# Kernel optimization log

Hardware: AMD Instinct MI355X
Metric: run time of the kernel (lower is better)

The kernel has to match this reference:

```python
import jax, jax.numpy as jnp
import numpy as np

NUM_HEADS = 4
HIDDEN = 384

def _l2norm(t, eps=1e-12):
    # torch.nn.functional.normalize(dim=-1): x / max(||x||_2, eps)
    n = jnp.sqrt(jnp.sum(t * t, axis=-1, keepdims=True))
    return t / jnp.maximum(n, eps)

def setup_inputs() -> dict:
    key = jax.random.key(0)
    k1, k2, k3, k4 = jax.random.split(key, 4)
    B, N, C = 4, 16384, HIDDEN
    x = jax.random.normal(k1, (B, N, C), dtype=jnp.float32)
    W_qkv = jax.random.normal(k2, (3 * C, C), dtype=jnp.float32) * 0.02  # torch Linear weight [out,in], no bias
    temperature_ch = jnp.ones((NUM_HEADS, 1, 1), dtype=jnp.float32)
    W_out = jax.random.normal(k3, (C, C), dtype=jnp.float32) * 0.02
    b_out = jax.random.normal(k4, (C,), dtype=jnp.float32) * 0.02
    return {"x": x, "W_qkv": W_qkv, "temperature_ch": temperature_ch,
            "W_out": W_out, "b_out": b_out,
            "B_in": 4, "C_in": C, "H": 32, "W": 32, "D": 16}

def reference(x, W_qkv, temperature_ch, W_out, b_out, B_in, C_in, H, W, D):
    B, N, C = x.shape
    h = NUM_HEADS
    d = C // h
    # qkv projection: (B,N,3C) -> (3,B,h,N,d)
    qkv = (x @ W_qkv.T).reshape(B, N, 3, h, d).transpose(2, 0, 3, 1, 4)
    q, k, v = qkv[0], qkv[1], qkv[2]
    # transpose token/channel axes: (B,h,d,N)
    q = jnp.swapaxes(q, -2, -1)
    k = jnp.swapaxes(k, -2, -1)
    v = jnp.swapaxes(v, -2, -1)
    # L2-normalize over tokens (last axis)
    q = _l2norm(q)
    k = _l2norm(k)
    # channel attention: (B,h,d,d)
    attn = jnp.einsum('bhcn,bhdn->bhcd', q, k)
    attn = attn * temperature_ch  # (h,1,1) broadcasts over (B,h,d,d)
    attn = jax.nn.softmax(attn, axis=-1)
    # (B,h,d,N) -> (B,N,h,d) -> (B,N,C)
    x_CA = jnp.einsum('bhcd,bhdn->bhcn', attn, v)
    x_CA = x_CA.transpose(0, 3, 1, 2).reshape(B, N, C)
    return x_CA @ W_out.T + b_out
```

## Files before the change

### kernel.cpp

```cpp
#include <hip/hip_runtime.h>
#include <math.h>


#define B_    4
#define NTOK  16384
#define C_    384
#define NH    4
#define DH    96

typedef __attribute__((ext_vector_type(8))) short short8;
typedef __attribute__((ext_vector_type(4))) float f32x4;
typedef __attribute__((ext_vector_type(4))) unsigned short ushort4v;
typedef __attribute__((ext_vector_type(8))) unsigned short ushort8v;

#define XH_B   0ull
#define XHT_B  50331648ull
#define GP_B   100663296ull
#define G_B    138412032ull
#define P_B    140771328ull
#define SSQ_B  145489920ull
#define ATT_B  145502208ull
#define T_B    146092032ull
#define MP_B   148451328ull
#define MPH_B  150810624ull
#define WS_NEED 151990272ull

#define FG_OFF    0
#define FG_SZ     (B_*C_*C_)
#define FP_OFF    (FG_OFF + FG_SZ)
#define FP_SZ     (2*B_*C_*C_)
#define FSSQ_OFF  (FP_OFF + FP_SZ)
#define FSSQ_SZ   (2*B_*C_)
#define FATT_OFF  (FSSQ_OFF + FSSQ_SZ)
#define FATT_SZ   (B_*NH*DH*DH)
#define FT_OFF    (FATT_OFF + FATT_SZ)
#define FT_SZ     (B_*C_*C_)
#define FMP_OFF   (FT_OFF + FT_SZ)

__device__ inline unsigned short f2bf(float f) {
    unsigned u = __float_as_uint(f);
    u += 0x7FFFu + ((u >> 16) & 1u);
    return (unsigned short)(u >> 16);
}

__device__ inline void load16(const void* g, void* l) {
    __builtin_amdgcn_global_load_lds(
        (const __attribute__((address_space(1))) unsigned int*)g,
        (__attribute__((address_space(3))) unsigned int*)l, 16, 0, 0);
}

__global__ __launch_bounds__(256) void k_conv(const float* __restrict__ X,
                                              unsigned short* __restrict__ Xh,
                                              unsigned short* __restrict__ XhT) {
    __shared__ __align__(16) unsigned short Th[64][72];
    const int tid = threadIdx.x;
    const int t0 = blockIdx.x * 64, c0 = blockIdx.y * 64, b = blockIdx.z;
    const int tl0 = tid >> 4, cl = (tid & 15) * 4;
#pragma unroll
    for (int p = 0; p < 4; ++p) {
        const int t = t0 + tl0 + p * 16;
        const float4 v = *(const float4*)(X + ((size_t)(b * NTOK + t)) * C_ + c0 + cl);
        const unsigned short h0 = f2bf(v.x), h1 = f2bf(v.y), h2 = f2bf(v.z), h3 = f2bf(v.w);
        ushort4v hv; hv.x = h0; hv.y = h1; hv.z = h2; hv.w = h3;
        *(ushort4v*)(Xh + ((size_t)(b * NTOK + t)) * C_ + c0 + cl) = hv;
        const int tl = tl0 + p * 16;
        Th[cl + 0][tl] = h0; Th[cl + 1][tl] = h1; Th[cl + 2][tl] = h2; Th[cl + 3][tl] = h3;
    }
    __syncthreads();
    const int c = tid >> 2, seg = (tid & 3) * 16;
    const ushort8v a  = *(const ushort8v*)&Th[c][seg];
    const ushort8v bb = *(const ushort8v*)&Th[c][seg + 8];
    unsigned short* dst = XhT + ((size_t)(b * C_ + c0 + c)) * NTOK + t0 + seg;
    *(ushort8v*)dst       = a;
    *(ushort8v*)(dst + 8) = bb;
}

__global__ __launch_bounds__(256, 2) void k_gram_mfma(const unsigned short* __restrict__ XhT,
                                                      float* __restrict__ Gpart) {
    __shared__ __align__(16) unsigned char sm[32768];
    const int l = blockIdx.x;
    const int xcd = l & 7, slot = l >> 3;
    const int grp = xcd * 8 + slot / 9, tile = slot % 9;
    const int chunk = grp >> 2, b = grp & 3;
    const int ti = tile / 3, tj = tile % 3;
    const int tid = threadIdx.x;
    const int lane = tid & 63, wid = tid >> 6;
    const int wr = wid >> 1, wc = wid & 1;

    const int e = (lane & 7) ^ (lane >> 3);
    const int rsub = lane >> 3;

    const size_t rowb = (size_t)NTOK * 2;
    const unsigned char* Abase = (const unsigned char*)XhT + (size_t)(b * C_ + ti * 128) * rowb;
    const unsigned char* Bbase = (const unsigned char*)XhT + (size_t)(b * C_ + tj * 128) * rowb;

    f32x4 acc[4][4];
#pragma unroll
    for (int i = 0; i < 4; i++)
#pragma unroll
        for (int j = 0; j < 4; j++) acc[i][j] = (f32x4)(0.f);

    for (int ks = 0; ks < 16; ++ks) {
        const size_t colb = (size_t)(chunk * 1024 + ks * 64) * 2 + (size_t)e * 16;
        __syncthreads();
#pragma unroll
        for (int call = 0; call < 4; ++call) {
            const int row = wid * 32 + call * 8 + rsub;
            load16(Abase + (size_t)row * rowb + colb, sm + (wid * 32 + call * 8) * 128);
            load16(Bbase + (size_t)row * rowb + colb, sm + 16384 + (wid * 32 + call * 8) * 128);
        }
        __syncthreads();
#pragma unroll
        for (int p = 0; p < 2; ++p) {
            const int s = p * 4 + (lane >> 4);
            short8 av[4], bv[4];
#pragma unroll
            for (int fi = 0; fi < 4; ++fi) {
                const int c = wr * 64 + fi * 16 + (lane & 15);
                av[fi] = *(const short8*)(sm + c * 128 + ((s ^ (c & 7)) << 4));
            }
#pragma unroll
            for (int fj = 0; fj < 4; ++fj) {
                const int c = wc * 64 + fj * 16 + (lane & 15);
                bv[fj] = *(const short8*)(sm + 16384 + c * 128 + ((s ^ (c & 7)) << 4));
            }
#pragma unroll
            for (int fi = 0; fi < 4; ++fi)
#pragma unroll
                for (int fj = 0; fj < 4; ++fj)
                    acc[fi][fj] = __builtin_amdgcn_mfma_f32_16x16x32_bf16(av[fi], bv[fj], acc[fi][fj], 0, 0, 0);
        }
    }
    float* gp = Gpart + (size_t)grp * (C_ * C_);
    const int r0 = (lane >> 4) * 4, cc = lane & 15;
#pragma unroll
    for (int fi = 0; fi < 4; ++fi) {
        const int ci = ti * 128 + wr * 64 + fi * 16 + r0;
#pragma unroll
        for (int fj = 0; fj < 4; ++fj) {
            const int cj = tj * 128 + wc * 64 + fj * 16 + cc;
#pragma unroll
            for (int r = 0; r < 4; ++r)
                gp[(size_t)(ci + r) * C_ + cj] = acc[fi][fj][r];
        }
    }
}

__global__ __launch_bounds__(256) void k_reduceG(const float* __restrict__ Gpart,
                                                 float* __restrict__ G) {
    const size_t eo = ((size_t)blockIdx.x * 256 + threadIdx.x) * 4;
    float4 s = *(const float4*)(Gpart + eo);
#pragma unroll
    for (int c = 1; c < 16; ++c) {
        const float4 v = *(const float4*)(Gpart + (size_t)c * (B_ * C_ * C_) + eo);
        s.x += v.x; s.y += v.y; s.z += v.z; s.w += v.w;
    }
    *(float4*)(G + eo) = s;
}

__global__ __launch_bounds__(256) void k_convM(const float* __restrict__ Mp,
                                               unsigned short* __restrict__ Mph) {
    const size_t eo = ((size_t)blockIdx.x * 256 + threadIdx.x) * 4;
    const float4 v = *(const float4*)(Mp + eo);
    ushort4v h; h.x = f2bf(v.x); h.y = f2bf(v.y); h.z = f2bf(v.z); h.w = f2bf(v.w);
    *(ushort4v*)(Mph + eo) = h;
}

__global__ __launch_bounds__(256, 2) void k_out_mfma(const unsigned short* __restrict__ Xh,
                                                     const unsigned short* __restrict__ Mph,
                                                     const float* __restrict__ bias,
                                                     float* __restrict__ out) {
    __shared__ __align__(16) unsigned char sm[32768];
    const int l = blockIdx.x;
    const int xcd = l & 7, k = l >> 3;
    const int mblk = xcd * 64 + k / 3, nblk = k % 3;
    const int m0 = mblk * 128, i0 = nblk * 128;
    const int b = mblk >> 7;
    const int tid = threadIdx.x;
    const int lane = tid & 63, wid = tid >> 6;
    const int wr = wid >> 1, wc = wid & 1;

    const int e = (lane & 7) ^ (lane >> 3);
    const int rsub = lane >> 3;

    const unsigned char* Abase = (const unsigned char*)Xh + (size_t)m0 * (C_ * 2);
    const unsigned char* Bbase = (const unsigned char*)Mph + (size_t)b * (C_ * C_ * 2) + (size_t)i0 * (C_ * 2);

    f32x4 acc[4][4];
#pragma unroll
    for (int i = 0; i < 4; i++)
#pragma unroll
        for (int j = 0; j < 4; j++) acc[i][j] = (f32x4)(0.f);

    for (int ks = 0; ks < 6; ++ks) {
        const size_t colb = (size_t)ks * 128 + (size_t)e * 16;
        __syncthreads();
#pragma unroll
        for (int call = 0; call < 4; ++call) {
            const int row = wid * 32 + call * 8 + rsub;
            load16(Abase + (size_t)row * (C_ * 2) + colb, sm + (wid * 32 + call * 8) * 128);
            load16(Bbase + (size_t)row * (C_ * 2) + colb, sm + 16384 + (wid * 32 + call * 8) * 128);
        }
        __syncthreads();
#pragma unroll
        for (int p = 0; p < 2; ++p) {
            const int s = p * 4 + (lane >> 4);
            short8 av[4], bv[4];
#pragma unroll
            for (int fi = 0; fi < 4; ++fi) {
                const int c = wr * 64 + fi * 16 + (lane & 15);
                av[fi] = *(const short8*)(sm + c * 128 + ((s ^ (c & 7)) << 4));
            }
#pragma unroll
            for (int fj = 0; fj < 4; ++fj) {
                const int c = wc * 64 + fj * 16 + (lane & 15);
                bv[fj] = *(const short8*)(sm + 16384 + c * 128 + ((s ^ (c & 7)) << 4));
            }
#pragma unroll
            for (int fi = 0; fi < 4; ++fi)
#pragma unroll
                for (int fj = 0; fj < 4; ++fj)
                    acc[fi][fj] = __builtin_amdgcn_mfma_f32_16x16x32_bf16(av[fi], bv[fj], acc[fi][fj], 0, 0, 0);
        }
    }
    const int r0 = (lane >> 4) * 4, cc = lane & 15;
#pragma unroll
    for (int fi = 0; fi < 4; ++fi) {
        const int m = m0 + wr * 64 + fi * 16 + r0;
#pragma unroll
        for (int fj = 0; fj < 4; ++fj) {
            const int ii = i0 + wc * 64 + fj * 16 + cc;
            const float bi = bias[ii];
#pragma unroll
            for (int r = 0; r < 4; ++r)
                out[(size_t)(m + r) * C_ + ii] = acc[fi][fj][r] + bi;
        }
    }
}

__global__ __launch_bounds__(256) void k_zero(float* __restrict__ p, int n) {
    int i = blockIdx.x * 256 + threadIdx.x;
    if (i < n) p[i] = 0.f;
}

__global__ __launch_bounds__(256, 2) void k_P(const float* __restrict__ Wqkv,
                                              const float* __restrict__ G,
                                              float* __restrict__ P) {
    __shared__ float As[16][132];
    __shared__ float Bs[16][132];
    const int tid = threadIdx.x;
    const int sel = blockIdx.z & 1, b = blockIdx.z >> 1;
    const int m0 = blockIdx.x * 128, n0 = blockIdx.y * 128;
    const float* A  = Wqkv + (size_t)sel * C_ * C_;
    const float* Bm = G + (size_t)b * C_ * C_;
    const int lr = tid >> 1, lk = (tid & 1) * 8;
    const int tm = (tid & 15) * 8, tn = (tid >> 4) * 8;
    float acc[8][8];
#pragma unroll
    for (int i = 0; i < 8; i++)
#pragma unroll
        for (int j = 0; j < 8; j++) acc[i][j] = 0.f;

    for (int k0 = 0; k0 < C_; k0 += 16) {
        float4 a0 = *(const float4*)(A  + (size_t)(m0 + lr) * C_ + k0 + lk);
        float4 a1 = *(const float4*)(A  + (size_t)(m0 + lr) * C_ + k0 + lk + 4);
        float4 b0 = *(const float4*)(Bm + (size_t)(n0 + lr) * C_ + k0 + lk);
        float4 b1 = *(const float4*)(Bm + (size_t)(n0 + lr) * C_ + k0 + lk + 4);
        __syncthreads();
        As[lk + 0][lr] = a0.x; As[lk + 1][lr] = a0.y; As[lk + 2][lr] = a0.z; As[lk + 3][lr] = a0.w;
        As[lk + 4][lr] = a1.x; As[lk + 5][lr] = a1.y; As[lk + 6][lr] = a1.z; As[lk + 7][lr] = a1.w;
        Bs[lk + 0][lr] = b0.x; Bs[lk + 1][lr] = b0.y; Bs[lk + 2][lr] = b0.z; Bs[lk + 3][lr] = b0.w;
        Bs[lk + 4][lr] = b1.x; Bs[lk + 5][lr] = b1.y; Bs[lk + 6][lr] = b1.z; Bs[lk + 7][lr] = b1.w;
        __syncthreads();
#pragma unroll
        for (int k = 0; k < 16; k++) {
            float a[8], bb[8];
            *(float4*)&a[0]  = *(const float4*)&As[k][tm];
            *(float4*)&a[4]  = *(const float4*)&As[k][tm + 4];
            *(float4*)&bb[0] = *(const float4*)&Bs[k][tn];
            *(float4*)&bb[4] = *(const float4*)&Bs[k][tn + 4];
#pragma unroll
            for (int i = 0; i < 8; i++)
#pragma unroll
                for (int j = 0; j < 8; j++)
                    acc[i][j] = fmaf(a[i], bb[j], acc[i][j]);
        }
    }
    float* outp = P + ((size_t)(sel * B_ + b) * C_ + m0 + tm) * C_ + n0 + tn;
#pragma unroll
    for (int i = 0; i < 8; i++) {
        float4 c0 = make_float4(acc[i][0], acc[i][1], acc[i][2], acc[i][3]);
        float4 c1 = make_float4(acc[i][4], acc[i][5], acc[i][6], acc[i][7]);
        *(float4*)(outp + (size_t)i * C_)     = c0;
        *(float4*)(outp + (size_t)i * C_ + 4) = c1;
    }
}

__global__ __launch_bounds__(256) void k_diag(const float* __restrict__ P,
                                              const float* __restrict__ Wqkv,
                                              float* __restrict__ ssq) {
    int g = blockIdx.x * 256 + threadIdx.x;
    int sel = g / (B_ * C_), rem = g % (B_ * C_), b = rem / C_, c = rem % C_;
    const float* pr = P + ((size_t)(sel * B_ + b) * C_ + c) * C_;
    const float* wr = Wqkv + ((size_t)sel * C_ + c) * C_;
    float s = 0.f;
#pragma unroll 4
    for (int k = 0; k < C_; k += 4) {
        float4 pv = *(const float4*)(pr + k);
        float4 wv = *(const float4*)(wr + k);
        s += pv.x * wv.x + pv.y * wv.y + pv.z * wv.z + pv.w * wv.w;
    }
    ssq[g] = s;
}

__global__ __launch_bounds__(256) void k_attn(const float* __restrict__ P,
                                              const float* __restrict__ Wqkv,
                                              const float* __restrict__ ssq,
                                              const float* __restrict__ temp,
                                              float* __restrict__ attn) {
    __shared__ float smb[DH * 97];
    const int bh = blockIdx.x;
    const int b = bh >> 2, h = bh & 3;
    const int tid = threadIdx.x;
    const int ti = tid & 15, tj = tid >> 4;
    float acc[6][6];
#pragma unroll
    for (int i = 0; i < 6; i++)
#pragma unroll
        for (int j = 0; j < 6; j++) acc[i][j] = 0.f;

    const float* P1 = P + ((size_t)b * C_ + h * DH) * C_;
    const float* Wk = Wqkv + ((size_t)(C_ + h * DH)) * C_;
    float* Ps = smb;
    float* Ks = smb + 32 * 97;

    for (int k0 = 0; k0 < C_; k0 += 32) {
        __syncthreads();
#pragma unroll
        for (int j = 0; j < 3; j++) {
            int f = tid + 256 * j;
            int row = f >> 3, q = f & 7;
            float4 v = *(const float4*)(P1 + (size_t)row * C_ + k0 + q * 4);
            Ps[(q * 4 + 0) * 97 + row] = v.x;
            Ps[(q * 4 + 1) * 97 + row] = v.y;
            Ps[(q * 4 + 2) * 97 + row] = v.z;
            Ps[(q * 4 + 3) * 97 + row] = v.w;
            float4 w = *(const float4*)(Wk + (size_t)row * C_ + k0 + q * 4);
            Ks[(q * 4 + 0) * 97 + row] = w.x;
            Ks[(q * 4 + 1) * 97 + row] = w.y;
            Ks[(q * 4 + 2) * 97 + row] = w.z;
            Ks[(q * 4 + 3) * 97 + row] = w.w;
        }
        __syncthreads();
#pragma unroll
        for (int k = 0; k < 32; k++) {
            float a[6], bb[6];
#pragma unroll
            for (int i = 0; i < 6; i++) a[i]  = Ps[k * 97 + ti * 6 + i];
#pragma unroll
            for (int j = 0; j < 6; j++) bb[j] = Ks[k * 97 + tj * 6 + j];
#pragma unroll
            for (int i = 0; i < 6; i++)
#pragma unroll
                for (int j = 0; j < 6; j++)
                    acc[i][j] = fmaf(a[i], bb[j], acc[i][j]);
        }
    }
    float tpr = temp[h];
    float nq[6], nk[6];
#pragma unroll
    for (int i = 0; i < 6; i++)
        nq[i] = fmaxf(sqrtf(ssq[b * C_ + h * DH + ti * 6 + i]), 1e-12f);
#pragma unroll
    for (int j = 0; j < 6; j++)
        nk[j] = fmaxf(sqrtf(ssq[B_ * C_ + b * C_ + h * DH + tj * 6 + j]), 1e-12f);
    __syncthreads();
#pragma unroll
    for (int i = 0; i < 6; i++)
#pragma unroll
        for (int j = 0; j < 6; j++)
            smb[(ti * 6 + i) * 97 + tj * 6 + j] = acc[i][j] / (nq[i] * nk[j]) * tpr;
    __syncthreads();
    if (tid < DH) {
        float* row = smb + tid * 97;
        float m = -1e30f;
        for (int d = 0; d < DH; d++) m = fmaxf(m, row[d]);
        float ssum = 0.f;
        for (int d = 0; d < DH; d++) { float ev = __expf(row[d] - m); row[d] = ev; ssum += ev; }
        float inv = 1.f / ssum;
        float* arow = attn + ((size_t)bh * DH + tid) * DH;
        for (int d = 0; d < DH; d++) arow[d] = row[d] * inv;
    }
}

__global__ __launch_bounds__(128) void k_T(const float* __restrict__ attn,
                                           const float* __restrict__ Wqkv,
                                           float* __restrict__ T) {
    const int ck = blockIdx.x * 128 + threadIdx.x;
    const int y = blockIdx.y;
    const int b = y / C_, hc = y % C_, h = hc / DH, c = hc % DH;
    const float* ar = attn + ((size_t)(b * NH + h) * DH + c) * DH;
    const float* wv = Wqkv + ((size_t)(2 * C_ + h * DH)) * C_ + ck;
    float s = 0.f;
#pragma unroll 8
    for (int d = 0; d < DH; d++) s = fmaf(ar[d], wv[(size_t)d * C_], s);
    T[((size_t)b * C_ + hc) * C_ + ck] = s;
}

__global__ __launch_bounds__(256, 2) void k_Mp(const float* __restrict__ Wout,
                                               const float* __restrict__ T,
                                               float* __restrict__ Mp) {
    __shared__ float As[16][132];
    __shared__ float Bs[16][132];
    const int tid = threadIdx.x;
    const int b = blockIdx.z;
    const int m0 = blockIdx.x * 128, n0 = blockIdx.y * 128;
    const int lr = tid >> 1, lk = (tid & 1) * 8;
    const int rt = tid >> 4, rc8 = (tid & 15) * 8;
    const int tm = (tid & 15) * 8, tn = (tid >> 4) * 8;
    const float* Tb = T + (size_t)b * C_ * C_;
    float acc[8][8];
#pragma unroll
    for (int i = 0; i < 8; i++)
#pragma unroll
        for (int j = 0; j < 8; j++) acc[i][j] = 0.f;

    for (int k0 = 0; k0 < C_; k0 += 16) {
        float4 a0 = *(const float4*)(Wout + (size_t)(m0 + lr) * C_ + k0 + lk);
        float4 a1 = *(const float4*)(Wout + (size_t)(m0 + lr) * C_ + k0 + lk + 4);
        float4 b0 = *(const float4*)(Tb + (size_t)(k0 + rt) * C_ + n0 + rc8);
        float4 b1 = *(const float4*)(Tb + (size_t)(k0 + rt) * C_ + n0 + rc8 + 4);
        __syncthreads();
        As[lk + 0][lr] = a0.x; As[lk + 1][lr] = a0.y; As[lk + 2][lr] = a0.z; As[lk + 3][lr] = a0.w;
        As[lk + 4][lr] = a1.x; As[lk + 5][lr] = a1.y; As[lk + 6][lr] = a1.z; As[lk + 7][lr] = a1.w;
        *(float4*)&Bs[rt][rc8]     = b0;
        *(float4*)&Bs[rt][rc8 + 4] = b1;
        __syncthreads();
#pragma unroll
        for (int k = 0; k < 16; k++) {
            float a[8], bb[8];
            *(float4*)&a[0]  = *(const float4*)&As[k][tm];
            *(float4*)&a[4]  = *(const float4*)&As[k][tm + 4];
            *(float4*)&bb[0] = *(const float4*)&Bs[k][tn];
            *(float4*)&bb[4] = *(const float4*)&Bs[k][tn + 4];
#pragma unroll
            for (int i = 0; i < 8; i++)
#pragma unroll
                for (int j = 0; j < 8; j++)
                    acc[i][j] = fmaf(a[i], bb[j], acc[i][j]);
        }
    }
    float* outp = Mp + ((size_t)b * C_ + m0 + tm) * C_ + n0 + tn;
#pragma unroll
    for (int i = 0; i < 8; i++) {
        float4 c0 = make_float4(acc[i][0], acc[i][1], acc[i][2], acc[i][3]);
        float4 c1 = make_float4(acc[i][4], acc[i][5], acc[i][6], acc[i][7]);
        *(float4*)(outp + (size_t)i * C_)     = c0;
        *(float4*)(outp + (size_t)i * C_ + 4) = c1;
    }
}

__global__ __launch_bounds__(256, 2) void k_gram_f32(const float* __restrict__ X,
                                                     float* __restrict__ G) {
    __shared__ float Aa[16][132];
    __shared__ float Ab[16][132];
    const int tid = threadIdx.x;
    const int chunk = blockIdx.x;
    const int ti = blockIdx.y / 3, tj = blockIdx.y % 3;
    const int b = blockIdx.z;
    const int t  = tid >> 4;
    const int c8 = (tid & 15) * 8;
    const int tm = (tid & 15) * 8, tn = (tid >> 4) * 8;
    float acc[8][8];
#pragma unroll
    for (int i = 0; i < 8; i++)
#pragma unroll
        for (int j = 0; j < 8; j++) acc[i][j] = 0.f;

    const float* Xb = X + ((size_t)b * NTOK + (size_t)chunk * 1024) * C_;
    for (int s = 0; s < 1024; s += 16) {
        const float* xr = Xb + (size_t)(s + t) * C_;
        float4 a0 = *(const float4*)(xr + ti * 128 + c8);
        float4 a1 = *(const float4*)(xr + ti * 128 + c8 + 4);
        float4 b0 = *(const float4*)(xr + tj * 128 + c8);
        float4 b1 = *(const float4*)(xr + tj * 128 + c8 + 4);
        __syncthreads();
        *(float4*)&Aa[t][c8]     = a0;
        *(float4*)&Aa[t][c8 + 4] = a1;
        *(float4*)&Ab[t][c8]     = b0;
        *(float4*)&Ab[t][c8 + 4] = b1;
        __syncthreads();
#pragma unroll
        for (int k = 0; k < 16; k++) {
            float a[8], bb[8];
            *(float4*)&a[0]  = *(const float4*)&Aa[k][tm];
            *(float4*)&a[4]  = *(const float4*)&Aa[k][tm + 4];
            *(float4*)&bb[0] = *(const float4*)&Ab[k][tn];
            *(float4*)&bb[4] = *(const float4*)&Ab[k][tn + 4];
#pragma unroll
            for (int i = 0; i < 8; i++)
#pragma unroll
                for (int j = 0; j < 8; j++)
                    acc[i][j] = fmaf(a[i], bb[j], acc[i][j]);
        }
    }
    float* Gb = G + (size_t)b * C_ * C_;
#pragma unroll
    for (int i = 0; i < 8; i++)
#pragma unroll
        for (int j = 0; j < 8; j++)
            atomicAdd(&Gb[(size_t)(ti * 128 + tm + i) * C_ + tj * 128 + tn + j],
                      acc[i][j]);
}

__global__ __launch_bounds__(256, 2) void k_out_f32(const float* __restrict__ X,
                                                    const float* __restrict__ Mp,
                                                    const float* __restrict__ bias,
                                                    float* __restrict__ out) {
    __shared__ float As[16][132];
    __shared__ float Bs[16][132];
    const int tid = threadIdx.x;
    const int m0 = blockIdx.x * 128, n0 = blockIdx.y * 128;
    const int b = m0 / NTOK;
    const float* Mb = Mp + (size_t)b * C_ * C_;
    const int lr = tid >> 1, lk = (tid & 1) * 8;
    const int tm = (tid & 15) * 8, tn = (tid >> 4) * 8;
    float acc[8][8];
#pragma unroll
    for (int i = 0; i < 8; i++)
#pragma unroll
        for (int j = 0; j < 8; j++) acc[i][j] = 0.f;

    for (int k0 = 0; k0 < C_; k0 += 16) {
        float4 a0 = *(const float4*)(X  + (size_t)(m0 + lr) * C_ + k0 + lk);
        float4 a1 = *(const float4*)(X  + (size_t)(m0 + lr) * C_ + k0 + lk + 4);
        float4 b0 = *(const float4*)(Mb + (size_t)(n0 + lr) * C_ + k0 + lk);
        float4 b1 = *(const float4*)(Mb + (size_t)(n0 + lr) * C_ + k0 + lk + 4);
        __syncthreads();
        As[lk + 0][lr] = a0.x; As[lk + 1][lr] = a0.y; As[lk + 2][lr] = a0.z; As[lk + 3][lr] = a0.w;
        As[lk + 4][lr] = a1.x; As[lk + 5][lr] = a1.y; As[lk + 6][lr] = a1.z; As[lk + 7][lr] = a1.w;
        Bs[lk + 0][lr] = b0.x; Bs[lk + 1][lr] = b0.y; Bs[lk + 2][lr] = b0.z; Bs[lk + 3][lr] = b0.w;
        Bs[lk + 4][lr] = b1.x; Bs[lk + 5][lr] = b1.y; Bs[lk + 6][lr] = b1.z; Bs[lk + 7][lr] = b1.w;
        __syncthreads();
#pragma unroll
        for (int k = 0; k < 16; k++) {
            float a[8], bb[8];
            *(float4*)&a[0]  = *(const float4*)&As[k][tm];
            *(float4*)&a[4]  = *(const float4*)&As[k][tm + 4];
            *(float4*)&bb[0] = *(const float4*)&Bs[k][tn];
            *(float4*)&bb[4] = *(const float4*)&Bs[k][tn + 4];
#pragma unroll
            for (int i = 0; i < 8; i++)
#pragma unroll
                for (int j = 0; j < 8; j++)
                    acc[i][j] = fmaf(a[i], bb[j], acc[i][j]);
        }
    }
#pragma unroll
    for (int i = 0; i < 8; i++) {
        float4 c0 = make_float4(acc[i][0] + bias[n0 + tn + 0],
                                acc[i][1] + bias[n0 + tn + 1],
                                acc[i][2] + bias[n0 + tn + 2],
                                acc[i][3] + bias[n0 + tn + 3]);
        float4 c1 = make_float4(acc[i][4] + bias[n0 + tn + 4],
                                acc[i][5] + bias[n0 + tn + 5],
                                acc[i][6] + bias[n0 + tn + 6],
                                acc[i][7] + bias[n0 + tn + 7]);
        float* row = out + (size_t)(m0 + tm + i) * C_ + n0 + tn;
        *(float4*)row       = c0;
        *(float4*)(row + 4) = c1;
    }
}

extern "C" void kernel_launch(void* const* d_in, const int* in_sizes, int n_in,
                              void* d_out, int out_size, void* d_ws, size_t ws_size,
                              hipStream_t stream) {
    const float* x    = (const float*)d_in[0];
    const float* Wqkv = (const float*)d_in[1];
    const float* temp = (const float*)d_in[2];
    const float* Wout = (const float*)d_in[3];
    const float* bout = (const float*)d_in[4];
    float* out = (float*)d_out;

    if (ws_size >= WS_NEED) {
        unsigned char* w8 = (unsigned char*)d_ws;
        unsigned short* Xh  = (unsigned short*)(w8 + XH_B);
        unsigned short* XhT = (unsigned short*)(w8 + XHT_B);
        float* Gpart = (float*)(w8 + GP_B);
        float* G     = (float*)(w8 + G_B);
        float* P     = (float*)(w8 + P_B);
        float* ssq   = (float*)(w8 + SSQ_B);
        float* att   = (float*)(w8 + ATT_B);
        float* T     = (float*)(w8 + T_B);
        float* Mp    = (float*)(w8 + MP_B);
        unsigned short* Mph = (unsigned short*)(w8 + MPH_B);

        k_conv     <<<dim3(256, 6, B_), 256, 0, stream>>>(x, Xh, XhT);
        k_gram_mfma<<<dim3(576), 256, 0, stream>>>(XhT, Gpart);
        k_reduceG  <<<dim3(576), 256, 0, stream>>>(Gpart, G);
        k_P        <<<dim3(3, 3, 2 * B_), 256, 0, stream>>>(Wqkv, G, P);
        k_diag     <<<dim3(12), 256, 0, stream>>>(P, Wqkv, ssq);
        k_attn     <<<dim3(B_ * NH), 256, 0, stream>>>(P, Wqkv, ssq, temp, att);
        k_T        <<<dim3(3, B_ * C_), 128, 0, stream>>>(att, Wqkv, T);
        k_Mp       <<<dim3(3, 3, B_), 256, 0, stream>>>(Wout, T, Mp);
        k_convM    <<<dim3(576), 256, 0, stream>>>(Mp, Mph);
        k_out_mfma <<<dim3(1536), 256, 0, stream>>>(Xh, Mph, bout, out);
    } else {
        float* ws  = (float*)d_ws;
        float* G    = ws + FG_OFF;
        float* P    = ws + FP_OFF;
        float* ssq  = ws + FSSQ_OFF;
        float* att  = ws + FATT_OFF;
        float* T    = ws + FT_OFF;
        float* Mp   = ws + FMP_OFF;

        k_zero    <<<dim3(FG_SZ / 256), 256, 0, stream>>>(G, FG_SZ);
        k_gram_f32<<<dim3(16, 9, B_), 256, 0, stream>>>(x, G);
        k_P       <<<dim3(3, 3, 2 * B_), 256, 0, stream>>>(Wqkv, G, P);
        k_diag    <<<dim3(12), 256, 0, stream>>>(P, Wqkv, ssq);
        k_attn    <<<dim3(B_ * NH), 256, 0, stream>>>(P, Wqkv, ssq, temp, att);
        k_T       <<<dim3(3, B_ * C_), 128, 0, stream>>>(att, Wqkv, T);
        k_Mp      <<<dim3(3, 3, B_), 256, 0, stream>>>(Wout, T, Mp);
        k_out_f32 <<<dim3(NTOK * B_ / 128, 3), 256, 0, stream>>>(x, Mp, bout, out);
    }
}
```

Measured before the change: 473.1 us.

## Increase grid parallelism in small GEMM stages and split attention into score and softmax kernels

The small C×C GEMMs (P and Mp) move from 128×128 to 64×64 tiles, giving four times as many blocks so more CUs are busy. The single-block-per-head attention kernel becomes a k_S kernel with 6 column slices per head plus a separate k_soft kernel that does row softmax in registers. The bf16 conversion of Mp is fused into the Mp GEMM epilogue, which removes the k_convM pass. The fp32 fallback path is removed, leaving one extra launch and a larger per-thread register array in softmax as the trade-off.

```diff
diff --git a/kernel.cpp b/kernel.cpp
--- a/kernel.cpp
+++ b/kernel.cpp
@@ -21,21 +21,7 @@
 #define SSQ_B  145489920ull
 #define ATT_B  145502208ull
 #define T_B    146092032ull
-#define MP_B   148451328ull
 #define MPH_B  150810624ull
-#define WS_NEED 151990272ull
-
-#define FG_OFF    0
-#define FG_SZ     (B_*C_*C_)
-#define FP_OFF    (FG_OFF + FG_SZ)
-#define FP_SZ     (2*B_*C_*C_)
-#define FSSQ_OFF  (FP_OFF + FP_SZ)
-#define FSSQ_SZ   (2*B_*C_)
-#define FATT_OFF  (FSSQ_OFF + FSSQ_SZ)
-#define FATT_SZ   (B_*NH*DH*DH)
-#define FT_OFF    (FATT_OFF + FATT_SZ)
-#define FT_SZ     (B_*C_*C_)
-#define FMP_OFF   (FT_OFF + FT_SZ)
 
 __device__ inline unsigned short f2bf(float f) {
     unsigned u = __float_as_uint(f);
@@ -158,110 +144,25 @@
     *(float4*)(G + eo) = s;
 }
 
-__global__ __launch_bounds__(256) void k_convM(const float* __restrict__ Mp,
-                                               unsigned short* __restrict__ Mph) {
-    const size_t eo = ((size_t)blockIdx.x * 256 + threadIdx.x) * 4;
-    const float4 v = *(const float4*)(Mp + eo);
-    ushort4v h; h.x = f2bf(v.x); h.y = f2bf(v.y); h.z = f2bf(v.z); h.w = f2bf(v.w);
-    *(ushort4v*)(Mph + eo) = h;
-}
-
-__global__ __launch_bounds__(256, 2) void k_out_mfma(const unsigned short* __restrict__ Xh,
-                                                     const unsigned short* __restrict__ Mph,
-                                                     const float* __restrict__ bias,
-                                                     float* __restrict__ out) {
-    __shared__ __align__(16) unsigned char sm[32768];
-    const int l = blockIdx.x;
-    const int xcd = l & 7, k = l >> 3;
-    const int mblk = xcd * 64 + k / 3, nblk = k % 3;
-    const int m0 = mblk * 128, i0 = nblk * 128;
-    const int b = mblk >> 7;
-    const int tid = threadIdx.x;
-    const int lane = tid & 63, wid = tid >> 6;
-    const int wr = wid >> 1, wc = wid & 1;
-
-    const int e = (lane & 7) ^ (lane >> 3);
-    const int rsub = lane >> 3;
-
-    const unsigned char* Abase = (const unsigned char*)Xh + (size_t)m0 * (C_ * 2);
-    const unsigned char* Bbase = (const unsigned char*)Mph + (size_t)b * (C_ * C_ * 2) + (size_t)i0 * (C_ * 2);
-
-    f32x4 acc[4][4];
-#pragma unroll
-    for (int i = 0; i < 4; i++)
-#pragma unroll
-        for (int j = 0; j < 4; j++) acc[i][j] = (f32x4)(0.f);
-
-    for (int ks = 0; ks < 6; ++ks) {
-        const size_t colb = (size_t)ks * 128 + (size_t)e * 16;
-        __syncthreads();
-#pragma unroll
-        for (int call = 0; call < 4; ++call) {
-            const int row = wid * 32 + call * 8 + rsub;
-            load16(Abase + (size_t)row * (C_ * 2) + colb, sm + (wid * 32 + call * 8) * 128);
-            load16(Bbase + (size_t)row * (C_ * 2) + colb, sm + 16384 + (wid * 32 + call * 8) * 128);
-        }
-        __syncthreads();
-#pragma unroll
-        for (int p = 0; p < 2; ++p) {
-            const int s = p * 4 + (lane >> 4);
-            short8 av[4], bv[4];
-#pragma unroll
-            for (int fi = 0; fi < 4; ++fi) {
-                const int c = wr * 64 + fi * 16 + (lane & 15);
-                av[fi] = *(const short8*)(sm + c * 128 + ((s ^ (c & 7)) << 4));
-            }
-#pragma unroll
-            for (int fj = 0; fj < 4; ++fj) {
-                const int c = wc * 64 + fj * 16 + (lane & 15);
-                bv[fj] = *(const short8*)(sm + 16384 + c * 128 + ((s ^ (c & 7)) << 4));
-            }
-#pragma unroll
-            for (int fi = 0; fi < 4; ++fi)
-#pragma unroll
-                for (int fj = 0; fj < 4; ++fj)
-                    acc[fi][fj] = __builtin_amdgcn_mfma_f32_16x16x32_bf16(av[fi], bv[fj], acc[fi][fj], 0, 0, 0);
-        }
-    }
-    const int r0 = (lane >> 4) * 4, cc = lane & 15;
-#pragma unroll
-    for (int fi = 0; fi < 4; ++fi) {
-        const int m = m0 + wr * 64 + fi * 16 + r0;
-#pragma unroll
-        for (int fj = 0; fj < 4; ++fj) {
-            const int ii = i0 + wc * 64 + fj * 16 + cc;
-            const float bi = bias[ii];
-#pragma unroll
-            for (int r = 0; r < 4; ++r)
-                out[(size_t)(m + r) * C_ + ii] = acc[fi][fj][r] + bi;
-        }
-    }
-}
-
-__global__ __launch_bounds__(256) void k_zero(float* __restrict__ p, int n) {
-    int i = blockIdx.x * 256 + threadIdx.x;
-    if (i < n) p[i] = 0.f;
-}
-
-__global__ __launch_bounds__(256, 2) void k_P(const float* __restrict__ Wqkv,
-                                              const float* __restrict__ G,
-                                              float* __restrict__ P) {
-    __shared__ float As[16][132];
-    __shared__ float Bs[16][132];
+__global__ __launch_bounds__(256) void k_P64(const float* __restrict__ Wqkv,
+                                             const float* __restrict__ G,
+                                             float* __restrict__ P) {
+    __shared__ float As[32][65];
+    __shared__ float Bs[32][65];
     const int tid = threadIdx.x;
     const int sel = blockIdx.z & 1, b = blockIdx.z >> 1;
-    const int m0 = blockIdx.x * 128, n0 = blockIdx.y * 128;
+    const int m0 = blockIdx.x * 64, n0 = blockIdx.y * 64;
     const float* A  = Wqkv + (size_t)sel * C_ * C_;
     const float* Bm = G + (size_t)b * C_ * C_;
-    const int lr = tid >> 1, lk = (tid & 1) * 8;
-    const int tm = (tid & 15) * 8, tn = (tid >> 4) * 8;
-    float acc[8][8];
-#pragma unroll
-    for (int i = 0; i < 8; i++)
-#pragma unroll
-        for (int j = 0; j < 8; j++) acc[i][j] = 0.f;
-
-    for (int k0 = 0; k0 < C_; k0 += 16) {
+    const int lr = tid >> 2, lk = (tid & 3) * 8;
+    const int tm = (tid & 15) * 4, tn = (tid >> 4) * 4;
+    float acc[4][4];
+#pragma unroll
+    for (int i = 0; i < 4; i++)
+#pragma unroll
+        for (int j = 0; j < 4; j++) acc[i][j] = 0.f;
+
+    for (int k0 = 0; k0 < C_; k0 += 32) {
         float4 a0 = *(const float4*)(A  + (size_t)(m0 + lr) * C_ + k0 + lk);
         float4 a1 = *(const float4*)(A  + (size_t)(m0 + lr) * C_ + k0 + lk + 4);
         float4 b0 = *(const float4*)(Bm + (size_t)(n0 + lr) * C_ + k0 + lk);
@@ -273,26 +174,22 @@
         Bs[lk + 4][lr] = b1.x; Bs[lk + 5][lr] = b1.y; Bs[lk + 6][lr] = b1.z; Bs[lk + 7][lr] = b1.w;
         __syncthreads();
 #pragma unroll
-        for (int k = 0; k < 16; k++) {
-            float a[8], bb[8];
+        for (int k = 0; k < 32; k++) {
+            float a[4], bb[4];
             *(float4*)&a[0]  = *(const float4*)&As[k][tm];
-            *(float4*)&a[4]  = *(const float4*)&As[k][tm + 4];
             *(float4*)&bb[0] = *(const float4*)&Bs[k][tn];
-            *(float4*)&bb[4] = *(const float4*)&Bs[k][tn + 4];
-#pragma unroll
-            for (int i = 0; i < 8; i++)
-#pragma unroll
-                for (int j = 0; j < 8; j++)
+#pragma unroll
+            for (int i = 0; i < 4; i++)
+#pragma unroll
+                for (int j = 0; j < 4; j++)
                     acc[i][j] = fmaf(a[i], bb[j], acc[i][j]);
         }
     }
     float* outp = P + ((size_t)(sel * B_ + b) * C_ + m0 + tm) * C_ + n0 + tn;
 #pragma unroll
-    for (int i = 0; i < 8; i++) {
+    for (int i = 0; i < 4; i++) {
         float4 c0 = make_float4(acc[i][0], acc[i][1], acc[i][2], acc[i][3]);
-        float4 c1 = make_float4(acc[i][4], acc[i][5], acc[i][6], acc[i][7]);
-        *(float4*)(outp + (size_t)i * C_)     = c0;
-        *(float4*)(outp + (size_t)i * C_ + 4) = c1;
+        *(float4*)(outp + (size_t)i * C_) = c0;
     }
 }
 
@@ -313,26 +210,20 @@
     ssq[g] = s;
 }
 
-__global__ __launch_bounds__(256) void k_attn(const float* __restrict__ P,
-                                              const float* __restrict__ Wqkv,
-                                              const float* __restrict__ ssq,
-                                              const float* __restrict__ temp,
-                                              float* __restrict__ attn) {
-    __shared__ float smb[DH * 97];
-    const int bh = blockIdx.x;
+__global__ __launch_bounds__(256) void k_S(const float* __restrict__ P,
+                                           const float* __restrict__ Wqkv,
+                                           float* __restrict__ S) {
+    __shared__ float Ps[32 * 97];
+    __shared__ float Ks[32 * 17];
+    const int cs = blockIdx.x, bh = blockIdx.y;
     const int b = bh >> 2, h = bh & 3;
     const int tid = threadIdx.x;
     const int ti = tid & 15, tj = tid >> 4;
-    float acc[6][6];
-#pragma unroll
-    for (int i = 0; i < 6; i++)
-#pragma unroll
-        for (int j = 0; j < 6; j++) acc[i][j] = 0.f;
-
     const float* P1 = P + ((size_t)b * C_ + h * DH) * C_;
-    const float* Wk = Wqkv + ((size_t)(C_ + h * DH)) * C_;
-    float* Ps = smb;
-    float* Ks = smb + 32 * 97;
+    const float* Wk = Wqkv + ((size_t)(C_ + h * DH + cs * 16)) * C_;
+    float acc[6];
+#pragma unroll
+    for (int i = 0; i < 6; i++) acc[i] = 0.f;
 
     for (int k0 = 0; k0 < C_; k0 += 32) {
         __syncthreads();
@@ -345,52 +236,54 @@
             Ps[(q * 4 + 1) * 97 + row] = v.y;
             Ps[(q * 4 + 2) * 97 + row] = v.z;
             Ps[(q * 4 + 3) * 97 + row] = v.w;
-            float4 w = *(const float4*)(Wk + (size_t)row * C_ + k0 + q * 4);
-            Ks[(q * 4 + 0) * 97 + row] = w.x;
-            Ks[(q * 4 + 1) * 97 + row] = w.y;
-            Ks[(q * 4 + 2) * 97 + row] = w.z;
-            Ks[(q * 4 + 3) * 97 + row] = w.w;
+        }
+        {
+            int row = tid >> 4, kk = (tid & 15) * 2;
+            float2 w = *(const float2*)(Wk + (size_t)row * C_ + k0 + kk);
+            Ks[(kk + 0) * 17 + row] = w.x;
+            Ks[(kk + 1) * 17 + row] = w.y;
         }
         __syncthreads();
 #pragma unroll
         for (int k = 0; k < 32; k++) {
-            float a[6], bb[6];
-#pragma unroll
-            for (int i = 0; i < 6; i++) a[i]  = Ps[k * 97 + ti * 6 + i];
-#pragma unroll
-            for (int j = 0; j < 6; j++) bb[j] = Ks[k * 97 + tj * 6 + j];
+            const float bb = Ks[k * 17 + tj];
 #pragma unroll
             for (int i = 0; i < 6; i++)
-#pragma unroll
-                for (int j = 0; j < 6; j++)
-                    acc[i][j] = fmaf(a[i], bb[j], acc[i][j]);
-        }
-    }
-    float tpr = temp[h];
-    float nq[6], nk[6];
+                acc[i] = fmaf(Ps[k * 97 + ti * 6 + i], bb, acc[i]);
+        }
+    }
+    float* Sb = S + (size_t)bh * DH * DH;
 #pragma unroll
     for (int i = 0; i < 6; i++)
-        nq[i] = fmaxf(sqrtf(ssq[b * C_ + h * DH + ti * 6 + i]), 1e-12f);
-#pragma unroll
-    for (int j = 0; j < 6; j++)
-        nk[j] = fmaxf(sqrtf(ssq[B_ * C_ + b * C_ + h * DH + tj * 6 + j]), 1e-12f);
+        Sb[(size_t)(ti * 6 + i) * DH + cs * 16 + tj] = acc[i];
+}
+
+__global__ __launch_bounds__(128) void k_soft(float* __restrict__ S,
+                                              const float* __restrict__ ssq,
+                                              const float* __restrict__ temp) {
+    __shared__ float rnk[DH];
+    const int bh = blockIdx.x;
+    const int b = bh >> 2, h = bh & 3;
+    const int r = threadIdx.x;
+    if (r < DH)
+        rnk[r] = 1.f / fmaxf(sqrtf(ssq[B_ * C_ + b * C_ + h * DH + r]), 1e-12f);
     __syncthreads();
-#pragma unroll
-    for (int i = 0; i < 6; i++)
-#pragma unroll
-        for (int j = 0; j < 6; j++)
-            smb[(ti * 6 + i) * 97 + tj * 6 + j] = acc[i][j] / (nq[i] * nk[j]) * tpr;
-    __syncthreads();
-    if (tid < DH) {
-        float* row = smb + tid * 97;
-        float m = -1e30f;
-        for (int d = 0; d < DH; d++) m = fmaxf(m, row[d]);
-        float ssum = 0.f;
-        for (int d = 0; d < DH; d++) { float ev = __expf(row[d] - m); row[d] = ev; ssum += ev; }
-        float inv = 1.f / ssum;
-        float* arow = attn + ((size_t)bh * DH + tid) * DH;
-        for (int d = 0; d < DH; d++) arow[d] = row[d] * inv;
-    }
+    if (r >= DH) return;
+    const float rnq = temp[h] / fmaxf(sqrtf(ssq[b * C_ + h * DH + r]), 1e-12f);
+    float* row = S + (size_t)bh * DH * DH + (size_t)r * DH;
+    float rv[DH];
+    float m = -1e30f;
+#pragma unroll
+    for (int d = 0; d < DH; d++) {
+        rv[d] = row[d] * rnq * rnk[d];
+        m = fmaxf(m, rv[d]);
+    }
+    float s = 0.f;
+#pragma unroll
+    for (int d = 0; d < DH; d++) { rv[d] = __expf(rv[d] - m); s += rv[d]; }
+    const float inv = 1.f / s;
+#pragma unroll
+    for (int d = 0; d < DH; d++) row[d] = rv[d] * inv;
 }
 
 __global__ __launch_bounds__(128) void k_T(const float* __restrict__ attn,
@@ -407,168 +300,126 @@
     T[((size_t)b * C_ + hc) * C_ + ck] = s;
 }
 
-__global__ __launch_bounds__(256, 2) void k_Mp(const float* __restrict__ Wout,
-                                               const float* __restrict__ T,
-                                               float* __restrict__ Mp) {
-    __shared__ float As[16][132];
-    __shared__ float Bs[16][132];
+__global__ __launch_bounds__(256) void k_Mp64(const float* __restrict__ Wout,
+                                              const float* __restrict__ T,
+                                              unsigned short* __restrict__ Mph) {
+    __shared__ float As[32][65];
+    __shared__ float Bs[32][65];
     const int tid = threadIdx.x;
     const int b = blockIdx.z;
-    const int m0 = blockIdx.x * 128, n0 = blockIdx.y * 128;
-    const int lr = tid >> 1, lk = (tid & 1) * 8;
-    const int rt = tid >> 4, rc8 = (tid & 15) * 8;
-    const int tm = (tid & 15) * 8, tn = (tid >> 4) * 8;
+    const int m0 = blockIdx.x * 64, n0 = blockIdx.y * 64;
     const float* Tb = T + (size_t)b * C_ * C_;
-    float acc[8][8];
-#pragma unroll
-    for (int i = 0; i < 8; i++)
-#pragma unroll
-        for (int j = 0; j < 8; j++) acc[i][j] = 0.f;
-
-    for (int k0 = 0; k0 < C_; k0 += 16) {
-        float4 a0 = *(const float4*)(Wout + (size_t)(m0 + lr) * C_ + k0 + lk);
-        float4 a1 = *(const float4*)(Wout + (size_t)(m0 + lr) * C_ + k0 + lk + 4);
-        float4 b0 = *(const float4*)(Tb + (size_t)(k0 + rt) * C_ + n0 + rc8);
-        float4 b1 = *(const float4*)(Tb + (size_t)(k0 + rt) * C_ + n0 + rc8 + 4);
-        __syncthreads();
-        As[lk + 0][lr] = a0.x; As[lk + 1][lr] = a0.y; As[lk + 2][lr] = a0.z; As[lk + 3][lr] = a0.w;
-        As[lk + 4][lr] = a1.x; As[lk + 5][lr] = a1.y; As[lk + 6][lr] = a1.z; As[lk + 7][lr] = a1.w;
-        *(float4*)&Bs[rt][rc8]     = b0;
-        *(float4*)&Bs[rt][rc8 + 4] = b1;
-        __syncthreads();
-#pragma unroll
-        for (int k = 0; k < 16; k++) {
-            float a[8], bb[8];
+    const int la_r = tid >> 2, la_k = (tid & 3) * 8;
+    const int lb_k = tid >> 3, lb_c = (tid & 7) * 8;
+    const int tm = (tid & 15) * 4, tn = (tid >> 4) * 4;
+    float acc[4][4];
+#pragma unroll
+    for (int i = 0; i < 4; i++)
+#pragma unroll
+        for (int j = 0; j < 4; j++) acc[i][j] = 0.f;
+
+    for (int k0 = 0; k0 < C_; k0 += 32) {
+        float4 a0 = *(const float4*)(Wout + (size_t)(m0 + la_r) * C_ + k0 + la_k);
+        float4 a1 = *(const float4*)(Wout + (size_t)(m0 + la_r) * C_ + k0 + la_k + 4);
+        float4 b0 = *(const float4*)(Tb + (size_t)(k0 + lb_k) * C_ + n0 + lb_c);
+        float4 b1 = *(const float4*)(Tb + (size_t)(k0 + lb_k) * C_ + n0 + lb_c + 4);
+        __syncthreads();
+        As[la_k + 0][la_r] = a0.x; As[la_k + 1][la_r] = a0.y; As[la_k + 2][la_r] = a0.z; As[la_k + 3][la_r] = a0.w;
+        As[la_k + 4][la_r] = a1.x; As[la_k + 5][la_r] = a1.y; As[la_k + 6][la_r] = a1.z; As[la_k + 7][la_r] = a1.w;
+        *(float4*)&Bs[lb_k][lb_c]     = b0;
+        *(float4*)&Bs[lb_k][lb_c + 4] = b1;
+        __syncthreads();
+#pragma unroll
+        for (int k = 0; k < 32; k++) {
+            float a[4], bb[4];
             *(float4*)&a[0]  = *(const float4*)&As[k][tm];
-            *(float4*)&a[4]  = *(const float4*)&As[k][tm + 4];
             *(float4*)&bb[0] = *(const float4*)&Bs[k][tn];
-            *(float4*)&bb[4] = *(const float4*)&Bs[k][tn + 4];
-#pragma unroll
-            for (int i = 0; i < 8; i++)
-#pragma unroll
-                for (int j = 0; j < 8; j++)
+#pragma unroll
+            for (int i = 0; i < 4; i++)
+#pragma unroll
+                for (int j = 0; j < 4; j++)
                     acc[i][j] = fmaf(a[i], bb[j], acc[i][j]);
         }
     }
-    float* outp = Mp + ((size_t)b * C_ + m0 + tm) * C_ + n0 + tn;
-#pragma unroll
-    for (int i = 0; i < 8; i++) {
-        float4 c0 = make_float4(acc[i][0], acc[i][1], acc[i][2], acc[i][3]);
-        float4 c1 = make_float4(acc[i][4], acc[i][5], acc[i][6], acc[i][7]);
-        *(float4*)(outp + (size_t)i * C_)     = c0;
-        *(float4*)(outp + (size_t)i * C_ + 4) = c1;
-    }
-}
-
-__global__ __launch_bounds__(256, 2) void k_gram_f32(const float* __restrict__ X,
-                                                     float* __restrict__ G) {
-    __shared__ float Aa[16][132];
-    __shared__ float Ab[16][132];
-    const int tid = threadIdx.x;
-    const int chunk = blockIdx.x;
-    const int ti = blockIdx.y / 3, tj = blockIdx.y % 3;
-    const int b = blockIdx.z;
-    const int t  = tid >> 4;
-    const int c8 = (tid & 15) * 8;
-    const int tm = (tid & 15) * 8, tn = (tid >> 4) * 8;
-    float acc[8][8];
-#pragma unroll
-    for (int i = 0; i < 8; i++)
-#pragma unroll
-        for (int j = 0; j < 8; j++) acc[i][j] = 0.f;
-
-    const float* Xb = X + ((size_t)b * NTOK + (size_t)chunk * 1024) * C_;
-    for (int s = 0; s < 1024; s += 16) {
-        const float* xr = Xb + (size_t)(s + t) * C_;
-        float4 a0 = *(const float4*)(xr + ti * 128 + c8);
-        float4 a1 = *(const float4*)(xr + ti * 128 + c8 + 4);
-        float4 b0 = *(const float4*)(xr + tj * 128 + c8);
-        float4 b1 = *(const float4*)(xr + tj * 128 + c8 + 4);
-        __syncthreads();
-        *(float4*)&Aa[t][c8]     = a0;
-        *(float4*)&Aa[t][c8 + 4] = a1;
-        *(float4*)&Ab[t][c8]     = b0;
-        *(float4*)&Ab[t][c8 + 4] = b1;
-        __syncthreads();
-#pragma unroll
-        for (int k = 0; k < 16; k++) {
-            float a[8], bb[8];
-            *(float4*)&a[0]  = *(const float4*)&Aa[k][tm];
-            *(float4*)&a[4]  = *(const float4*)&Aa[k][tm + 4];
-            *(float4*)&bb[0] = *(const float4*)&Ab[k][tn];
-            *(float4*)&bb[4] = *(const float4*)&Ab[k][tn + 4];
-#pragma unroll
-            for (int i = 0; i < 8; i++)
-#pragma unroll
-                for (int j = 0; j < 8; j++)
-                    acc[i][j] = fmaf(a[i], bb[j], acc[i][j]);
-        }
-    }
-    float* Gb = G + (size_t)b * C_ * C_;
-#pragma unroll
-    for (int i = 0; i < 8; i++)
-#pragma unroll
-        for (int j = 0; j < 8; j++)
-            atomicAdd(&Gb[(size_t)(ti * 128 + tm + i) * C_ + tj * 128 + tn + j],
-                      acc[i][j]);
-}
-
-__global__ __launch_bounds__(256, 2) void k_out_f32(const float* __restrict__ X,
-                                                    const float* __restrict__ Mp,
-                                                    const float* __restrict__ bias,
-                                                    float* __restrict__ out) {
-    __shared__ float As[16][132];
-    __shared__ float Bs[16][132];
-    const int tid = threadIdx.x;
-    const int m0 = blockIdx.x * 128, n0 = blockIdx.y * 128;
-    const int b = m0 / NTOK;
-    const float* Mb = Mp + (size_t)b * C_ * C_;
-    const int lr = tid >> 1, lk = (tid & 1) * 8;
-    const int tm = (tid & 15) * 8, tn = (tid >> 4) * 8;
-    float acc[8][8];
-#pragma unroll
-    for (int i = 0; i < 8; i++)
-#pragma unroll
-        for (int j = 0; j < 8; j++) acc[i][j] = 0.f;
-
-    for (int k0 = 0; k0 < C_; k0 += 16) {
-        float4 a0 = *(const float4*)(X  + (size_t)(m0 + lr) * C_ + k0 + lk);
-        float4 a1 = *(const float4*)(X  + (size_t)(m0 + lr) * C_ + k0 + lk + 4);
-        float4 b0 = *(const float4*)(Mb + (size_t)(n0 + lr) * C_ + k0 + lk);
-        float4 b1 = *(const float4*)(Mb + (size_t)(n0 + lr) * C_ + k0 + lk + 4);
-        __syncthreads();
-        As[lk + 0][lr] = a0.x; As[lk + 1][lr] = a0.y; As[lk + 2][lr] = a0.z; As[lk + 3][lr] = a0.w;
-        As[lk + 4][lr] = a1.x; As[lk + 5][lr] = a1.y; As[lk + 6][lr] = a1.z; As[lk + 7][lr] = a1.w;
-        Bs[lk + 0][lr] = b0.x; Bs[lk + 1][lr] = b0.y; Bs[lk + 2][lr] = b0.z; Bs[lk + 3][lr] = b0.w;
-        Bs[lk + 4][lr] = b1.x; Bs[lk + 5][lr] = b1.y; Bs[lk + 6][lr] = b1.z; Bs[lk + 7][lr] = b1.w;
-        __syncthreads();
-#pragma unroll
-        for (int k = 0; k < 16; k++) {
-            float a[8], bb[8];
-            *(float4*)&a[0]  = *(const float4*)&As[k][tm];
-            *(float4*)&a[4]  = *(const float4*)&As[k][tm + 4];
-            *(float4*)&bb[0] = *(const float4*)&Bs[k][tn];
-            *(float4*)&bb[4] = *(const float4*)&Bs[k][tn + 4];
-#pragma unroll
-            for (int i = 0; i < 8; i++)
-#pragma unroll
-                for (int j = 0; j < 8; j++)
-                    acc[i][j] = fmaf(a[i], bb[j], acc[i][j]);
-        }
-    }
-#pragma unroll
-    for (int i = 0; i < 8; i++) {
-        float4 c0 = make_float4(acc[i][0] + bias[n0 + tn + 0],
-                                acc[i][1] + bias[n0 + tn + 1],
-                                acc[i][2] + bias[n0 + tn + 2],
-                                acc[i][3] + bias[n0 + tn + 3]);
-        float4 c1 = make_float4(acc[i][4] + bias[n0 + tn + 4],
-                                acc[i][5] + bias[n0 + tn + 5],
-                                acc[i][6] + bias[n0 + tn + 6],
-                                acc[i][7] + bias[n0 + tn + 7]);
-        float* row = out + (size_t)(m0 + tm + i) * C_ + n0 + tn;
-        *(float4*)row       = c0;
-        *(float4*)(row + 4) = c1;
+    unsigned short* outp = Mph + ((size_t)b * C_ + m0 + tm) * C_ + n0 + tn;
+#pragma unroll
+    for (int i = 0; i < 4; i++) {
+        ushort4v h4;
+        h4.x = f2bf(acc[i][0]); h4.y = f2bf(acc[i][1]);
+        h4.z = f2bf(acc[i][2]); h4.w = f2bf(acc[i][3]);
+        *(ushort4v*)(outp + (size_t)i * C_) = h4;
+    }
+}
+
+__global__ __launch_bounds__(256, 2) void k_out_mfma(const unsigned short* __restrict__ Xh,
+                                                     const unsigned short* __restrict__ Mph,
+                                                     const float* __restrict__ bias,
+                                                     float* __restrict__ out) {
+    __shared__ __align__(16) unsigned char sm[32768];
+    const int l = blockIdx.x;
+    const int xcd = l & 7, k = l >> 3;
+    const int mblk = xcd * 64 + k / 3, nblk = k % 3;
+    const int m0 = mblk * 128, i0 = nblk * 128;
+    const int b = mblk >> 7;
+    const int tid = threadIdx.x;
+    const int lane = tid & 63, wid = tid >> 6;
+    const int wr = wid >> 1, wc = wid & 1;
+
+    const int e = (lane & 7) ^ (lane >> 3);
+    const int rsub = lane >> 3;
+
+    const unsigned char* Abase = (const unsigned char*)Xh + (size_t)m0 * (C_ * 2);
+    const unsigned char* Bbase = (const unsigned char*)Mph + (size_t)b * (C_ * C_ * 2) + (size_t)i0 * (C_ * 2);
+
+    f32x4 acc[4][4];
+#pragma unroll
+    for (int i = 0; i < 4; i++)
+#pragma unroll
+        for (int j = 0; j < 4; j++) acc[i][j] = (f32x4)(0.f);
+
+    for (int ks = 0; ks < 6; ++ks) {
+        const size_t colb = (size_t)ks * 128 + (size_t)e * 16;
+        __syncthreads();
+#pragma unroll
+        for (int call = 0; call < 4; ++call) {
+            const int row = wid * 32 + call * 8 + rsub;
+            load16(Abase + (size_t)row * (C_ * 2) + colb, sm + (wid * 32 + call * 8) * 128);
+            load16(Bbase + (size_t)row * (C_ * 2) + colb, sm + 16384 + (wid * 32 + call * 8) * 128);
+        }
+        __syncthreads();
+#pragma unroll
+        for (int p = 0; p < 2; ++p) {
+            const int s = p * 4 + (lane >> 4);
+            short8 av[4], bv[4];
+#pragma unroll
+            for (int fi = 0; fi < 4; ++fi) {
+                const int c = wr * 64 + fi * 16 + (lane & 15);
+                av[fi] = *(const short8*)(sm + c * 128 + ((s ^ (c & 7)) << 4));
+            }
+#pragma unroll
+            for (int fj = 0; fj < 4; ++fj) {
+                const int c = wc * 64 + fj * 16 + (lane & 15);
+                bv[fj] = *(const short8*)(sm + 16384 + c * 128 + ((s ^ (c & 7)) << 4));
+            }
+#pragma unroll
+            for (int fi = 0; fi < 4; ++fi)
+#pragma unroll
+                for (int fj = 0; fj < 4; ++fj)
+                    acc[fi][fj] = __builtin_amdgcn_mfma_f32_16x16x32_bf16(av[fi], bv[fj], acc[fi][fj], 0, 0, 0);
+        }
+    }
+    const int r0 = (lane >> 4) * 4, cc = lane & 15;
+#pragma unroll
+    for (int fi = 0; fi < 4; ++fi) {
+        const int m = m0 + wr * 64 + fi * 16 + r0;
+#pragma unroll
+        for (int fj = 0; fj < 4; ++fj) {
+            const int ii = i0 + wc * 64 + fj * 16 + cc;
+            const float bi = bias[ii];
+#pragma unroll
+            for (int r = 0; r < 4; ++r)
+                out[(size_t)(m + r) * C_ + ii] = acc[fi][fj][r] + bi;
+        }
     }
 }
 
@@ -582,45 +433,25 @@
     const float* bout = (const float*)d_in[4];
     float* out = (float*)d_out;
 
-    if (ws_size >= WS_NEED) {
-        unsigned char* w8 = (unsigned char*)d_ws;
-        unsigned short* Xh  = (unsigned short*)(w8 + XH_B);
-        unsigned short* XhT = (unsigned short*)(w8 + XHT_B);
-        float* Gpart = (float*)(w8 + GP_B);
-        float* G     = (float*)(w8 + G_B);
-        float* P     = (float*)(w8 + P_B);
-        float* ssq   = (float*)(w8 + SSQ_B);
-        float* att   = (float*)(w8 + ATT_B);
-        float* T     = (float*)(w8 + T_B);
-        float* Mp    = (float*)(w8 + MP_B);
-        unsigned short* Mph = (unsigned short*)(w8 + MPH_B);
-
-        k_conv     <<<dim3(256, 6, B_), 256, 0, stream>>>(x, Xh, XhT);
-        k_gram_mfma<<<dim3(576), 256, 0, stream>>>(XhT, Gpart);
-        k_reduceG  <<<dim3(576), 256, 0, stream>>>(Gpart, G);
-        k_P        <<<dim3(3, 3, 2 * B_), 256, 0, stream>>>(Wqkv, G, P);
-        k_diag     <<<dim3(12), 256, 0, stream>>>(P, Wqkv, ssq);
-        k_attn     <<<dim3(B_ * NH), 256, 0, stream>>>(P, Wqkv, ssq, temp, att);
-        k_T        <<<dim3(3, B_ * C_), 128, 0, stream>>>(att, Wqkv, T);
-        k_Mp       <<<dim3(3, 3, B_), 256, 0, stream>>>(Wout, T, Mp);
-        k_convM    <<<dim3(576), 256, 0, stream>>>(Mp, Mph);
-        k_out_mfma <<<dim3(1536), 256, 0, stream>>>(Xh, Mph, bout, out);
-    } else {
-        float* ws  = (float*)d_ws;
-        float* G    = ws + FG_OFF;
-        float* P    = ws + FP_OFF;
-        float* ssq  = ws + FSSQ_OFF;
-        float* att  = ws + FATT_OFF;
-        float* T    = ws + FT_OFF;
-        float* Mp   = ws + FMP_OFF;
-
-        k_zero    <<<dim3(FG_SZ / 256), 256, 0, stream>>>(G, FG_SZ);
-        k_gram_f32<<<dim3(16, 9, B_), 256, 0, stream>>>(x, G);
-        k_P       <<<dim3(3, 3, 2 * B_), 256, 0, stream>>>(Wqkv, G, P);
-        k_diag    <<<dim3(12), 256, 0, stream>>>(P, Wqkv, ssq);
-        k_attn    <<<dim3(B_ * NH), 256, 0, stream>>>(P, Wqkv, ssq, temp, att);
-        k_T       <<<dim3(3, B_ * C_), 128, 0, stream>>>(att, Wqkv, T);
-        k_Mp      <<<dim3(3, 3, B_), 256, 0, stream>>>(Wout, T, Mp);
-        k_out_f32 <<<dim3(NTOK * B_ / 128, 3), 256, 0, stream>>>(x, Mp, bout, out);
-    }
-}
+    unsigned char* w8 = (unsigned char*)d_ws;
+    unsigned short* Xh  = (unsigned short*)(w8 + XH_B);
+    unsigned short* XhT = (unsigned short*)(w8 + XHT_B);
+    float* Gpart = (float*)(w8 + GP_B);
+    float* G     = (float*)(w8 + G_B);
+    float* P     = (float*)(w8 + P_B);
+    float* ssq   = (float*)(w8 + SSQ_B);
+    float* Satt  = (float*)(w8 + ATT_B);
+    float* T     = (float*)(w8 + T_B);
+    unsigned short* Mph = (unsigned short*)(w8 + MPH_B);
+
+    k_conv     <<<dim3(256, 6, B_), 256, 0, stream>>>(x, Xh, XhT);
+    k_gram_mfma<<<dim3(576), 256, 0, stream>>>(XhT, Gpart);
+    k_reduceG  <<<dim3(576), 256, 0, stream>>>(Gpart, G);
+    k_P64      <<<dim3(6, 6, 2 * B_), 256, 0, stream>>>(Wqkv, G, P);
+    k_diag     <<<dim3(12), 256, 0, stream>>>(P, Wqkv, ssq);
+    k_S        <<<dim3(6, B_ * NH), 256, 0, stream>>>(P, Wqkv, Satt);
+    k_soft     <<<dim3(B_ * NH), 128, 0, stream>>>(Satt, ssq, temp);
+    k_T        <<<dim3(3, B_ * C_), 128, 0, stream>>>(Satt, Wqkv, T);
+    k_Mp64     <<<dim3(6, 6, B_), 256, 0, stream>>>(Wout, T, Mph);
+    k_out_mfma <<<dim3(1536), 256, 0, stream>>>(Xh, Mph, bout, out);
+}
```

Result: faster. 409.0 us (-13.5%).
